# Kernel optimization log

Measured on AMD Instinct MI355X. Metric: run time of the kernel, lower is better.

Reference implementation:

```python
import jax, jax.numpy as jnp
import numpy as np
import math

NH = 16
SIGMA = 1.5
KS = 7


def _gaussian_blur_16x16(x):
    # x: (N, 16, 16); torchvision GaussianBlur(7, 1.5) with reflect padding
    hx = jnp.arange(KS, dtype=x.dtype) - (KS - 1) / 2.0
    k1 = jnp.exp(-0.5 * (hx / SIGMA) ** 2)
    k1 = k1 / k1.sum()
    k2 = jnp.outer(k1, k1)[None, None]  # (1,1,7,7)
    pad = KS // 2
    xp = jnp.pad(x, ((0, 0), (pad, pad), (pad, pad)), mode='reflect')[:, None]
    y = jax.lax.conv_general_dilated(xp, k2, (1, 1), 'VALID')
    return y[:, 0]


def _normalize(w):
    mn, mx = w.min(), w.max()
    return (w - mn) / (mx - mn)


def _blurred_map(f, b_perm):
    # f, b_perm: (B, 256, 256)
    B = f.shape[0]
    bi = f * b_perm
    bi = bi.reshape(B * 256, 16, 16)
    bl = _gaussian_blur_16x16(bi)
    bl = jnp.clip(_normalize(bl), 0.0, 1.0)
    bl = bl.reshape(B, 256, 256)
    return bl * f * b_perm


def setup_inputs() -> dict:
    key = jax.random.key(0)
    ks = jax.random.split(key, 16)
    B, T, C = 4, 827, 1024
    inp = {
        'x': jax.random.normal(ks[0], (B, T, C), jnp.float32),
        'h': jax.random.normal(ks[1], (B, NH, 827, 827), jnp.float32) * 0.1,
        'f01': jax.random.uniform(ks[2], (B, 256, 256), jnp.float32),
        'f02': jax.random.uniform(ks[3], (B, 256, 256), jnp.float32),
        'f12': jax.random.uniform(ks[4], (B, 256, 256), jnp.float32),
        'b01': jax.random.uniform(ks[5], (B, 256, 256), jnp.float32),
        'b02': jax.random.uniform(ks[6], (B, 256, 256), jnp.float32),
        'b12': jax.random.uniform(ks[7], (B, 256, 256), jnp.float32),
        'Wq': jax.random.normal(ks[8], (C, C), jnp.float32) * 0.02,
        'bq': jnp.zeros((C,), jnp.float32),
        'Wk': jax.random.normal(ks[9], (C, C), jnp.float32) * 0.02,
        'bk': jnp.zeros((C,), jnp.float32),
        'Wv': jax.random.normal(ks[10], (C, C), jnp.float32) * 0.02,
        'bv': jnp.zeros((C,), jnp.float32),
        'Wp': jax.random.normal(ks[11], (C, C), jnp.float32) * 0.02,
        'bp': jnp.zeros((C,), jnp.float32),
    }
    return inp


def reference(x, h, f01, f02, f12, b01, b02, b12,
              Wq, bq, Wk, bk, Wv, bv, Wp, bp):
    B, T, C = x.shape
    hd = C // NH
    # QKV projections -> (B, NH, T, hd)
    def proj(W, b):
        return (x @ W + b).reshape(B, T, NH, hd).transpose(0, 2, 1, 3)
    q, k, v = proj(Wq, bq), proj(Wk, bk), proj(Wv, bv)

    att = jnp.einsum('bhtd,bhsd->bhts', q, k) * (1.0 / math.sqrt(hd))
    att = h[:, :, :T, :T] + att  # adaptive additive bias

    # bidirectional epipolar multiplicative masks with blur
    b01p = jnp.transpose(b01, (0, 2, 1))
    b02p = jnp.transpose(b02, (0, 2, 1))
    b12p = jnp.transpose(b12, (0, 2, 1))
    blur01 = _blurred_map(f01, b01p)[:, None]  # (B,1,256,256), broadcast over heads
    blur02 = _blurred_map(f02, b02p)[:, None]
    blur12 = _blurred_map(f12, b12p)[:, None]

    n1 = min(T - 285, 256)
    att = att.at[:, :, 285:285 + n1, 0:256].multiply(blur01[:, :, :n1])
    if T > 571:
        n2 = T - 571
        att = att.at[:, :, 571:T, 0:256].multiply(blur02[:, :, :n2])
        att = att.at[:, :, 571:T, 286:542].multiply(blur12[:, :, :n2])

    mask = jnp.tril(jnp.ones((T, T), dtype=bool))
    att = jnp.where(mask, att, -jnp.inf)
    att = jax.nn.softmax(att, axis=-1)

    y = jnp.einsum('bhts,bhsd->bhtd', att, v)
    y = y.transpose(0, 2, 1, 3).reshape(B, T, C)
    return y @ Wp + bp
```

## Files before the change

### kernel.cpp

```cpp
#include <hip/hip_runtime.h>
#include <math.h>

using bfrag8 = __attribute__((ext_vector_type(8))) short;
using facc4  = __attribute__((ext_vector_type(4))) float;

#define MFMA16(a,b,c) __builtin_amdgcn_mfma_f32_16x16x32_bf16((a),(b),(c),0,0,0)

#define T_SEQ 827
#define T_PAD 832
#define NHEAD 16
#define NEG_INF (-__builtin_inff())
#define CM_TOT 1179392

static __device__ __forceinline__ unsigned short f2bf(float f) {
    unsigned int x = __float_as_uint(f);
    unsigned int r = x + 0x7FFFu + ((x >> 16) & 1u);
    return (unsigned short)(r >> 16);
}

static __device__ __forceinline__ void gl16(const void* g, void* l) {
    __builtin_amdgcn_global_load_lds(
        (const __attribute__((address_space(1))) unsigned int*)g,
        (__attribute__((address_space(3))) unsigned int*)l,
        16, 0, 0);
}

__global__ __launch_bounds__(256) void k_front(const float* __restrict__ x,
                                               unsigned short* __restrict__ x_bf,
                                               float* __restrict__ cm,
                                               unsigned short* q, unsigned short* k,
                                               unsigned short* vT,
                                               const float* __restrict__ Wq,
                                               const float* __restrict__ Wk,
                                               const float* __restrict__ Wv,
                                               const float* __restrict__ Wp,
                                               unsigned short* __restrict__ Wt_out,
                                               const float* f01, const float* f02, const float* f12,
                                               const float* b01, const float* b02, const float* b12,
                                               float* __restrict__ bl,
                                               float* __restrict__ pmm) {
    __shared__ float tile[32][33];
    __shared__ float img[16][17], tmp[16][17];
    __shared__ float smn[4], smx[4];
    int bid = blockIdx.x, tid = threadIdx.x;

    if (bid < 3308) {
        int i = (bid * 256 + tid) * 4;
        float4 v = *reinterpret_cast<const float4*>(x + i);
        ushort4 o;
        o.x = f2bf(v.x); o.y = f2bf(v.y); o.z = f2bf(v.z); o.w = f2bf(v.w);
        *reinterpret_cast<ushort4*>(x_bf + i) = o;
    } else if (bid < 4460) {
        int base = (bid - 3308) * 1024 + tid * 4;
        if (base + 4 <= CM_TOT) {
            float4 one = {1.f, 1.f, 1.f, 1.f};
            *reinterpret_cast<float4*>(cm + base) = one;
        } else {
#pragma unroll
            for (int j = 0; j < 4; ++j)
                if (base + j < CM_TOT) cm[base + j] = 1.f;
        }
    } else if (bid < 4524) {
        int bh = bid - 4460;
        for (int i = tid; i < 320; i += 256) {
            int t = 827 + i / 64, d = i % 64;
            q[((size_t)bh * T_PAD + t) * 64 + d] = 0;
            k[((size_t)bh * T_PAD + t) * 64 + d] = 0;
        }
        for (int i = tid; i < 4096; i += 256) {
            int d = i >> 6, s = 768 + (i & 63);
            vT[((size_t)bh * 64 + d) * T_PAD + s] = 0;
        }
    } else if (bid < 8620) {
        int i = bid - 4524;
        int z = i >> 10, rem = i & 1023;
        int bx = rem & 31, by = rem >> 5;
        const float* W = (z == 0) ? Wq : (z == 1) ? Wk : (z == 2) ? Wv : Wp;
        unsigned short* Wt = Wt_out + (size_t)z * 1048576;
        int tx = tid & 31, ty0 = tid >> 5;
#pragma unroll
        for (int j = 0; j < 4; ++j) {
            int ty = ty0 + j * 8;
            tile[ty][tx] = W[(size_t)(by * 32 + ty) * 1024 + bx * 32 + tx];
        }
        __syncthreads();
#pragma unroll
        for (int j = 0; j < 4; ++j) {
            int ty = ty0 + j * 8;
            Wt[(size_t)(bx * 32 + ty) * 1024 + by * 32 + tx] = f2bf(tile[tx][ty]);
        }
    } else {
        int i = bid - 8620;
        int m = i >> 10, rem = i & 1023, b = rem >> 8, r = rem & 255;
        const float* f  = (m == 0) ? f01 : (m == 1) ? f02 : f12;
        const float* bm = (m == 0) ? b01 : (m == 1) ? b02 : b12;
        int ii = tid >> 4, j = tid & 15;

        float k1[7]; float ks = 0.f;
#pragma unroll
        for (int d = 0; d < 7; ++d) { float hx = (float)d - 3.f; k1[d] = expf(-0.5f * hx * hx / 2.25f); ks += k1[d]; }
#pragma unroll
        for (int d = 0; d < 7; ++d) k1[d] /= ks;

        size_t idx = (size_t)b * 65536 + (size_t)r * 256 + tid;
        float bi = f[idx] * bm[(size_t)b * 65536 + (size_t)tid * 256 + r];
        img[ii][j] = bi;
        __syncthreads();
        float ha = 0.f;
#pragma unroll
        for (int d = 0; d < 7; ++d) { int p = j - 3 + d; p = p < 0 ? -p : (p > 15 ? 30 - p : p); ha += k1[d] * img[ii][p]; }
        tmp[ii][j] = ha;
        __syncthreads();
        float v = 0.f;
#pragma unroll
        for (int d = 0; d < 7; ++d) { int p = ii - 3 + d; p = p < 0 ? -p : (p > 15 ? 30 - p : p); v += k1[d] * tmp[p][j]; }
        bl[(size_t)m * 262144 + idx] = v;

        float mn = v, mx = v;
#pragma unroll
        for (int off = 32; off; off >>= 1) { mn = fminf(mn, __shfl_xor(mn, off)); mx = fmaxf(mx, __shfl_xor(mx, off)); }
        int wid = tid >> 6, lane = tid & 63;
        if (lane == 0) { smn[wid] = mn; smx[wid] = mx; }
        __syncthreads();
        if (tid == 0) {
            mn = fminf(fminf(smn[0], smn[1]), fminf(smn[2], smn[3]));
            mx = fmaxf(fmaxf(smx[0], smx[1]), fmaxf(smx[2], smx[3]));
            pmm[2 * i]     = mn;
            pmm[2 * i + 1] = mx;
        }
    }
}

__global__ __launch_bounds__(256) void k_gemm_qkv(const unsigned short* __restrict__ A,
                                              const unsigned short* __restrict__ Bt,
                                              const float* __restrict__ b0, const float* __restrict__ b1,
                                              const float* __restrict__ b2,
                                              unsigned short* __restrict__ qo, unsigned short* __restrict__ ko,
                                              unsigned short* __restrict__ vo, int M,
                                              const float* f01, const float* f02, const float* f12,
                                              const float* b01, const float* b02, const float* b12,
                                              const float* __restrict__ bl,
                                              const float* __restrict__ pmm,
                                              float* __restrict__ cm) {
    __shared__ unsigned short As[2][4096];
    __shared__ unsigned short Bs[2][4096];
    int bid = blockIdx.x, tid = threadIdx.x;

    if (bid >= 624) {
        int i = bid - 624;
        int m = i >> 10, rem = i & 1023, b = rem >> 8, r = rem & 255;
        float mn = __builtin_inff(), mx = 0.f;
        for (int kk = tid; kk < 1024; kk += 256) {
            int e = m * 1024 + kk;
            mn = fminf(mn, pmm[2 * e]);
            mx = fmaxf(mx, pmm[2 * e + 1]);
        }
#pragma unroll
        for (int off = 32; off; off >>= 1) { mn = fminf(mn, __shfl_xor(mn, off)); mx = fmaxf(mx, __shfl_xor(mx, off)); }
        float* fs = reinterpret_cast<float*>(&As[0][0]);
        int wid = tid >> 6, lane = tid & 63;
        if (lane == 0) { fs[wid] = mn; fs[4 + wid] = mx; }
        __syncthreads();
        mn = fminf(fminf(fs[0], fs[1]), fminf(fs[2], fs[3]));
        mx = fmaxf(fmaxf(fs[4], fs[5]), fmaxf(fs[6], fs[7]));

        const float* f  = (m == 0) ? f01 : (m == 1) ? f02 : f12;
        const float* bm = (m == 0) ? b01 : (m == 1) ? b02 : b12;
        size_t idx = (size_t)b * 65536 + (size_t)r * 256 + tid;
        float w = (bl[(size_t)m * 262144 + idx] - mn) / (mx - mn);
        w = fminf(fmaxf(w, 0.f), 1.f);
        float val = w * f[idx] * bm[(size_t)b * 65536 + (size_t)tid * 256 + r];
        int row = (m == 0) ? r : r + 286;
        int col = (m == 2) ? tid + 286 : tid;
        cm[((size_t)b * 542 + row) * 544 + col] = val;
        return;
    }

    int swz = (bid & 7) * 78 + (bid >> 3);
    int m0 = (swz % 26) * 128, n0 = (swz / 26) * 128;
    int wid = tid >> 6, lane = tid & 63;
    int g = lane >> 4, l15 = lane & 15;
    int wm = wid >> 1, wn = wid & 1;
    facc4 acc[4][4] = {};

    int ar0 = m0 + (tid >> 2); if (ar0 > M - 1) ar0 = M - 1;
    int ar1 = m0 + 64 + (tid >> 2); if (ar1 > M - 1) ar1 = M - 1;
    const unsigned short* Ap0 = A + (size_t)ar0 * 1024 + (tid & 3) * 8;
    const unsigned short* Ap1 = A + (size_t)ar1 * 1024 + (tid & 3) * 8;
    const unsigned short* Bp0 = Bt + (size_t)(n0 + (tid >> 2)) * 1024 + (tid & 3) * 8;
    const unsigned short* Bp1 = Bp0 + (size_t)64 * 1024;

    auto stage = [&](int koff, int buf) {
        gl16(Ap0 + koff, &As[buf][0] + (wid << 9));
        gl16(Ap1 + koff, &As[buf][0] + (wid << 9) + 2048);
        gl16(Bp0 + koff, &Bs[buf][0] + (wid << 9));
        gl16(Bp1 + koff, &Bs[buf][0] + (wid << 9) + 2048);
    };

    stage(0, 0);
    for (int k0 = 0; k0 < 32; ++k0) {
        int cur = k0 & 1;
        bool morek = (k0 + 1 < 32);
        if (morek) {
            stage((k0 + 1) * 32, cur ^ 1);
            asm volatile("s_waitcnt vmcnt(4)" ::: "memory");
        } else {
            asm volatile("s_waitcnt vmcnt(0)" ::: "memory");
        }
        __builtin_amdgcn_s_barrier();
        __builtin_amdgcn_sched_barrier(0);

        bfrag8 af[4], bf[4];
#pragma unroll
        for (int mi = 0; mi < 4; ++mi)
            af[mi] = *reinterpret_cast<const bfrag8*>(&As[cur][(wm * 64 + mi * 16 + l15) * 32 + g * 8]);
#pragma unroll
        for (int ni = 0; ni < 4; ++ni)
            bf[ni] = *reinterpret_cast<const bfrag8*>(&Bs[cur][(wn * 64 + ni * 16 + l15) * 32 + g * 8]);
        __builtin_amdgcn_s_setprio(1);
#pragma unroll
        for (int mi = 0; mi < 4; ++mi)
#pragma unroll
            for (int ni = 0; ni < 4; ++ni)
                acc[mi][ni] = MFMA16(af[mi], bf[ni], acc[mi][ni]);
        __builtin_amdgcn_s_setprio(0);

        __builtin_amdgcn_sched_barrier(0);
        if (morek) __builtin_amdgcn_s_barrier();
    }

    int which = n0 >> 10;
    const float* bb = (which == 0 ? b0 : (which == 1 ? b1 : b2));
#pragma unroll
    for (int mi = 0; mi < 4; ++mi)
#pragma unroll
        for (int ni = 0; ni < 4; ++ni)
#pragma unroll
            for (int r = 0; r < 4; ++r) {
                int row = m0 + wm * 64 + mi * 16 + g * 4 + r;
                if (row >= M) continue;
                int col = n0 + wn * 64 + ni * 16 + l15;
                float v = acc[mi][ni][r] + bb[col & 1023];
                int b = row / T_SEQ, t = row - b * T_SEQ;
                int cc = col & 1023;
                int hh = cc >> 6, d = cc & 63;
                size_t bh = (size_t)(b * NHEAD + hh);
                if (which == 0) {
                    qo[(bh * T_PAD + t) * 64 + d] = f2bf(v);
                } else if (which == 1) {
                    int du = (((d >> 3) ^ (t & 7)) << 3) | (d & 7);
                    ko[(bh * T_PAD + t) * 64 + du] = f2bf(v);
                } else {
                    int sl = t & 63;
                    int su = (((sl >> 3) ^ (d & 7)) << 3) | (t & 7);
                    vo[(bh * 64 + d) * T_PAD + (t - sl) + su] = f2bf(v);
                }
            }
}

__global__ __launch_bounds__(256) void k_proj64(const unsigned short* __restrict__ A,
                                                const unsigned short* __restrict__ Bt,
                                                const float* __restrict__ bias,
                                                float* __restrict__ out, int M) {
    __shared__ unsigned short As[2048];
    __shared__ unsigned short Bs[2048];
    int bid = blockIdx.x, tid = threadIdx.x;
    int swz = (bid & 7) * 104 + (bid >> 3);
    int m0 = (swz % 52) * 64, n0 = (swz / 52) * 64;
    int wid = tid >> 6, lane = tid & 63;
    int g = lane >> 4, l15 = lane & 15;
    int wm = wid >> 1, wn = wid & 1;
    facc4 acc[2][2] = {};

    int ar = m0 + (tid >> 2); if (ar > M - 1) ar = M - 1;
    const unsigned short* Ap = A + (size_t)ar * 1024 + (tid & 3) * 8;
    const unsigned short* Bp = Bt + (size_t)(n0 + (tid >> 2)) * 1024 + (tid & 3) * 8;
    unsigned short* asw = As + (wid << 9);
    unsigned short* bsw = Bs + (wid << 9);

    for (int k0 = 0; k0 < 1024; k0 += 32) {
        if (k0) __syncthreads();
        gl16(Ap + k0, asw);
        gl16(Bp + k0, bsw);
        __syncthreads();
        bfrag8 af[2], bf[2];
#pragma unroll
        for (int mi = 0; mi < 2; ++mi)
            af[mi] = *reinterpret_cast<const bfrag8*>(&As[(wm * 32 + mi * 16 + l15) * 32 + g * 8]);
#pragma unroll
        for (int ni = 0; ni < 2; ++ni)
            bf[ni] = *reinterpret_cast<const bfrag8*>(&Bs[(wn * 32 + ni * 16 + l15) * 32 + g * 8]);
#pragma unroll
        for (int mi = 0; mi < 2; ++mi)
#pragma unroll
            for (int ni = 0; ni < 2; ++ni)
                acc[mi][ni] = MFMA16(af[mi], bf[ni], acc[mi][ni]);
    }

#pragma unroll
    for (int mi = 0; mi < 2; ++mi)
#pragma unroll
        for (int ni = 0; ni < 2; ++ni)
#pragma unroll
            for (int r = 0; r < 4; ++r) {
                int row = m0 + wm * 32 + mi * 16 + g * 4 + r;
                if (row >= M) continue;
                int col = n0 + wn * 32 + ni * 16 + l15;
                out[(size_t)row * 1024 + col] = acc[mi][ni][r] + bias[col];
            }
}

__global__ __launch_bounds__(256) void k_attn(const unsigned short* __restrict__ qb,
                                              const unsigned short* __restrict__ kb,
                                              const unsigned short* __restrict__ vT,
                                              const float* __restrict__ h,
                                              const float* __restrict__ cm,
                                              unsigned short* __restrict__ y) {
    int blk0 = blockIdx.x;
    int blk = (blk0 & 7) * 104 + (blk0 >> 3);
    int bh = blk / 13;
    int qt = 12 - (blk % 13);
    int b = bh >> 4, hh = bh & 15;
    int tid = threadIdx.x, wid = tid >> 6, lane = tid & 63;
    int g = lane >> 4, l15 = lane & 15;
    int t0 = qt * 64 + wid * 16;
    int t = t0 + l15;
    int tcl = t > 826 ? 826 : t;
    int ntiles = qt + 1;

    __shared__ unsigned short Ks[2][4096];
    __shared__ unsigned short Vs[2][4096];
    __shared__ unsigned short Ps[4][1024];
    unsigned short* pw = &Ps[wid][0];

    const unsigned short* Kbase = kb + (size_t)bh * T_PAD * 64;
    const unsigned short* Vbase = vT + (size_t)bh * 64 * T_PAD;
    const float* hrow = h + (size_t)bh * T_SEQ * T_SEQ + (size_t)tcl * T_SEQ;
    int rt = t - 285; rt = rt < 0 ? 0 : (rt > 541 ? 541 : rt);
    const float* cmrow = cm + ((size_t)b * 542 + rt) * 544;
    bool tm = (t >= 285);

    size_t qrow = ((size_t)bh * T_PAD + t) * 64 + g * 8;
    bfrag8 aq0 = *reinterpret_cast<const bfrag8*>(qb + qrow);
    bfrag8 aq1 = *reinterpret_cast<const bfrag8*>(qb + qrow + 32);

    auto stage = [&](int s0, int buf) {
        const unsigned short* kt = Kbase + (size_t)s0 * 64;
        unsigned short* kd = &Ks[buf][0] + (wid << 9);
        gl16(kt + tid * 8, kd);
        gl16(kt + 2048 + tid * 8, kd + 2048);
        const unsigned short* vt = Vbase + s0;
        unsigned short* vd = &Vs[buf][0] + (wid << 9);
        gl16(vt + (size_t)(tid >> 3) * T_PAD + (tid & 7) * 8, vd);
        gl16(vt + (size_t)((tid >> 3) + 32) * T_PAD + (tid & 7) * 8, vd + 2048);
    };

    auto loadh = [&](int s0t, float* hv, float* mv) {
#pragma unroll
        for (int nt = 0; nt < 4; ++nt) {
            int sb = s0t + nt * 16 + 4 * g;
            float h4[4];
            if (sb + 3 <= tcl) {
                __builtin_memcpy(h4, hrow + sb, 16);
            } else {
#pragma unroll
                for (int j = 0; j < 4; ++j) {
                    float hx = 0.f;
                    if (sb + j <= tcl) hx = hrow[sb + j];
                    h4[j] = hx;
                }
            }
            float m4[4];
            if (tm && sb <= 540) {
                __builtin_memcpy(m4, cmrow + sb, 16);
            } else {
#pragma unroll
                for (int j = 0; j < 4; ++j) m4[j] = 1.f;
            }
#pragma unroll
            for (int j = 0; j < 4; ++j) { hv[nt * 4 + j] = h4[j]; mv[nt * 4 + j] = m4[j]; }
        }
    };

    float m_r = NEG_INF, l_r = 0.f;
    facc4 acc[4] = {};
    float hv[16], mv[16];
    loadh(0, hv, mv);
    stage(0, 0);

    for (int it = 0; it < ntiles; ++it) {
        int cur = it & 1, s0 = it * 64;
        bool more = (it + 1 < ntiles);
        bool diag = !more;
        __syncthreads();
        if (more) stage(s0 + 64, cur ^ 1);

        facc4 sf[4] = {};
        __builtin_amdgcn_s_setprio(1);
#pragma unroll
        for (int nt = 0; nt < 4; ++nt) {
            int row = nt * 16 + l15;
            const unsigned short* kp = &Ks[cur][row * 64];
            bfrag8 k0 = *reinterpret_cast<const bfrag8*>(kp + ((g ^ (row & 7)) << 3));
            bfrag8 k1 = *reinterpret_cast<const bfrag8*>(kp + (((4 + g) ^ (row & 7)) << 3));
            sf[nt] = MFMA16(k0, aq0, sf[nt]);
            sf[nt] = MFMA16(k1, aq1, sf[nt]);
        }
        __builtin_amdgcn_s_setprio(0);

        float vmax = NEG_INF;
#pragma unroll
        for (int nt = 0; nt < 4; ++nt)
#pragma unroll
            for (int r = 0; r < 4; ++r) {
                float val = fmaf(sf[nt][r], 0.125f, hv[nt * 4 + r]) * mv[nt * 4 + r];
                if (diag) {
                    int s = s0 + nt * 16 + 4 * g + r;
                    val = (s <= tcl) ? val : NEG_INF;
                }
                sf[nt][r] = val;
                vmax = fmaxf(vmax, val);
            }

        if (more) loadh(s0 + 64, hv, mv);

        vmax = fmaxf(vmax, __shfl_xor(vmax, 16));
        vmax = fmaxf(vmax, __shfl_xor(vmax, 32));

        bool noresc = __all(vmax <= m_r + 6.0f);
        float mnew = fmaxf(m_r, vmax);
        float mexp = noresc ? m_r : mnew;

        float ps = 0.f;
#pragma unroll
        for (int nt = 0; nt < 4; ++nt)
#pragma unroll
            for (int r = 0; r < 4; ++r) {
                float p = __expf(sf[nt][r] - mexp);
                sf[nt][r] = p;
                ps += p;
            }
        ps += __shfl_xor(ps, 16);
        ps += __shfl_xor(ps, 32);

#pragma unroll
        for (int nt = 0; nt < 4; ++nt) {
            unsigned u0, u1;
            asm("v_cvt_pk_bf16_f32 %0, %1, %2" : "=v"(u0) : "v"(sf[nt][0]), "v"(sf[nt][1]));
            asm("v_cvt_pk_bf16_f32 %0, %1, %2" : "=v"(u1) : "v"(sf[nt][2]), "v"(sf[nt][3]));
            int el = (l15 * 64 + nt * 16 + 4 * g) ^ ((l15 & 7) << 3);
            uint2 uu; uu.x = u0; uu.y = u1;
            *reinterpret_cast<uint2*>(&pw[el]) = uu;
        }

        if (!noresc) {
            float scale = __expf(m_r - mnew);
            l_r = l_r * scale + ps;
#pragma unroll
            for (int r = 0; r < 4; ++r) {
                float sc = __int_as_float(__builtin_amdgcn_ds_bpermute((4 * g + r) * 4, __float_as_int(scale)));
#pragma unroll
                for (int dt = 0; dt < 4; ++dt) acc[dt][r] *= sc;
            }
            m_r = mnew;
        } else {
            l_r += ps;
        }

        __builtin_amdgcn_s_setprio(1);
#pragma unroll
        for (int c2 = 0; c2 < 2; ++c2) {
            int ela = (l15 * 64 + c2 * 32 + 8 * g) ^ ((l15 & 7) << 3);
            bfrag8 ap = *reinterpret_cast<const bfrag8*>(&pw[ela]);
#pragma unroll
            for (int dt = 0; dt < 4; ++dt) {
                int row = dt * 16 + l15;
                bfrag8 vf = *reinterpret_cast<const bfrag8*>(&Vs[cur][row * 64 + (((c2 * 4 + g) ^ (row & 7)) << 3)]);
                acc[dt] = MFMA16(ap, vf, acc[dt]);
            }
        }
        __builtin_amdgcn_s_setprio(0);
    }

    float linv = 1.0f / l_r;
#pragma unroll
    for (int r = 0; r < 4; ++r) {
        float li = __int_as_float(__builtin_amdgcn_ds_bpermute((4 * g + r) * 4, __float_as_int(linv)));
        int tt = t0 + 4 * g + r;
        if (tt < T_SEQ) {
#pragma unroll
            for (int dt = 0; dt < 4; ++dt)
                y[((size_t)(b * T_SEQ) + tt) * 1024 + hh * 64 + dt * 16 + l15] = f2bf(acc[dt][r] * li);
        }
    }
}

extern "C" void kernel_launch(void* const* d_in, const int* in_sizes, int n_in,
                              void* d_out, int out_size, void* d_ws, size_t ws_size,
                              hipStream_t stream) {
    const float* x   = (const float*)d_in[0];
    const float* h   = (const float*)d_in[1];
    const float* f01 = (const float*)d_in[2];
    const float* f02 = (const float*)d_in[3];
    const float* f12 = (const float*)d_in[4];
    const float* b01 = (const float*)d_in[5];
    const float* b02 = (const float*)d_in[6];
    const float* b12 = (const float*)d_in[7];
    const float* Wq  = (const float*)d_in[8];
    const float* bq  = (const float*)d_in[9];
    const float* Wk  = (const float*)d_in[10];
    const float* bk  = (const float*)d_in[11];
    const float* Wv  = (const float*)d_in[12];
    const float* bv  = (const float*)d_in[13];
    const float* Wp  = (const float*)d_in[14];
    const float* bp  = (const float*)d_in[15];

    char* ws = (char*)d_ws;
    float* pmm    = (float*)(ws + 256);
    float* bl     = (float*)(ws + 256 + 24576);
    float* cmb    = (float*)(ws + 256 + 24576 + 3145728);
    unsigned short* x_bf  = (unsigned short*)(ws + 256 + 24576 + 3145728 + 4717568);
    unsigned short* WtQKV = x_bf + (size_t)3308 * 1024;
    unsigned short* WtP   = WtQKV + (size_t)3072 * 1024;
    unsigned short* q_bf  = WtP + (size_t)1024 * 1024;
    unsigned short* k_bf  = q_bf + (size_t)64 * T_PAD * 64;
    unsigned short* vTb   = k_bf + (size_t)64 * T_PAD * 64;
    unsigned short* y_bf  = vTb  + (size_t)64 * T_PAD * 64;

    k_front<<<11692, 256, 0, stream>>>(x, x_bf, cmb, q_bf, k_bf, vTb,
                                       Wq, Wk, Wv, Wp, WtQKV,
                                       f01, f02, f12, b01, b02, b12, bl, pmm);
    k_gemm_qkv<<<3696, 256, 0, stream>>>(x_bf, WtQKV, bq, bk, bv, q_bf, k_bf, vTb, 3308,
                                         f01, f02, f12, b01, b02, b12, bl, pmm, cmb);
    k_attn<<<832, 256, 0, stream>>>(q_bf, k_bf, vTb, h, cmb, y_bf);
    k_proj64<<<832, 256, 0, stream>>>(y_bf, WtP, bp, (float*)d_out, 3308);
}
```

Measured before the change: 133.3 us.

## Split long causal attention query tiles across two blocks with a combine pass

For query tiles 7-12, the attention kernel now splits the key range into two halves, each processed by its own block. The partial accumulators and running max/sum are written to workspace and merged flash-decoding style in a new k_combine kernel. This balances the triangular causal workload and raises the block count from 832 to 1216 to shorten the tail. In exchange it adds an extra launch, fp32 partial-result traffic, and reuse of the x_bf and bl workspace regions as scratch.

New measurement: 135.9 us. No clear change (+2.0%).

```diff
diff --git a/kernel.cpp b/kernel.cpp
--- a/kernel.cpp
+++ b/kernel.cpp
@@ -315,18 +315,29 @@
                                               const unsigned short* __restrict__ vT,
                                               const float* __restrict__ h,
                                               const float* __restrict__ cm,
-                                              unsigned short* __restrict__ y) {
+                                              unsigned short* __restrict__ y,
+                                              float* __restrict__ pacc,
+                                              float* __restrict__ pml) {
     int blk0 = blockIdx.x;
-    int blk = (blk0 & 7) * 104 + (blk0 >> 3);
-    int bh = blk / 13;
-    int qt = 12 - (blk % 13);
+    int swz = (blk0 & 7) * 152 + (blk0 >> 3);
+    int bh = swz / 19, j = swz % 19;
+    int qt, itlo, ithi, pidx = -1;
+    if (j < 7) {
+        qt = j; itlo = 0; ithi = qt + 1;
+    } else {
+        qt = 7 + ((j - 7) >> 1);
+        int half = (j - 7) & 1;
+        int h0 = (qt + 2) >> 1;
+        itlo = half ? h0 : 0;
+        ithi = half ? (qt + 1) : h0;
+        pidx = bh * 12 + (qt - 7) * 2 + half;
+    }
     int b = bh >> 4, hh = bh & 15;
     int tid = threadIdx.x, wid = tid >> 6, lane = tid & 63;
     int g = lane >> 4, l15 = lane & 15;
     int t0 = qt * 64 + wid * 16;
     int t = t0 + l15;
     int tcl = t > 826 ? 826 : t;
-    int ntiles = qt + 1;
 
     __shared__ unsigned short Ks[2][4096];
     __shared__ unsigned short Vs[2][4096];
@@ -364,10 +375,10 @@
                 __builtin_memcpy(h4, hrow + sb, 16);
             } else {
 #pragma unroll
-                for (int j = 0; j < 4; ++j) {
+                for (int jj = 0; jj < 4; ++jj) {
                     float hx = 0.f;
-                    if (sb + j <= tcl) hx = hrow[sb + j];
-                    h4[j] = hx;
+                    if (sb + jj <= tcl) hx = hrow[sb + jj];
+                    h4[jj] = hx;
                 }
             }
             float m4[4];
@@ -375,23 +386,23 @@
                 __builtin_memcpy(m4, cmrow + sb, 16);
             } else {
 #pragma unroll
-                for (int j = 0; j < 4; ++j) m4[j] = 1.f;
-            }
-#pragma unroll
-            for (int j = 0; j < 4; ++j) { hv[nt * 4 + j] = h4[j]; mv[nt * 4 + j] = m4[j]; }
+                for (int jj = 0; jj < 4; ++jj) m4[jj] = 1.f;
+            }
+#pragma unroll
+            for (int jj = 0; jj < 4; ++jj) { hv[nt * 4 + jj] = h4[jj]; mv[nt * 4 + jj] = m4[jj]; }
         }
     };
 
     float m_r = NEG_INF, l_r = 0.f;
     facc4 acc[4] = {};
     float hv[16], mv[16];
-    loadh(0, hv, mv);
-    stage(0, 0);
-
-    for (int it = 0; it < ntiles; ++it) {
-        int cur = it & 1, s0 = it * 64;
-        bool more = (it + 1 < ntiles);
-        bool diag = !more;
+    loadh(itlo * 64, hv, mv);
+    stage(itlo * 64, 0);
+
+    for (int it = itlo; it < ithi; ++it) {
+        int cur = (it - itlo) & 1, s0 = it * 64;
+        bool more = (it + 1 < ithi);
+        bool diag = (it == qt);
         __syncthreads();
         if (more) stage(s0 + 64, cur ^ 1);
 
@@ -482,16 +493,62 @@
         __builtin_amdgcn_s_setprio(0);
     }
 
-    float linv = 1.0f / l_r;
-#pragma unroll
-    for (int r = 0; r < 4; ++r) {
-        float li = __int_as_float(__builtin_amdgcn_ds_bpermute((4 * g + r) * 4, __float_as_int(linv)));
-        int tt = t0 + 4 * g + r;
-        if (tt < T_SEQ) {
-#pragma unroll
-            for (int dt = 0; dt < 4; ++dt)
-                y[((size_t)(b * T_SEQ) + tt) * 1024 + hh * 64 + dt * 16 + l15] = f2bf(acc[dt][r] * li);
-        }
+    if (pidx < 0) {
+        float linv = 1.0f / l_r;
+#pragma unroll
+        for (int r = 0; r < 4; ++r) {
+            float li = __int_as_float(__builtin_amdgcn_ds_bpermute((4 * g + r) * 4, __float_as_int(linv)));
+            int tt = t0 + 4 * g + r;
+            if (tt < T_SEQ) {
+#pragma unroll
+                for (int dt = 0; dt < 4; ++dt)
+                    y[((size_t)(b * T_SEQ) + tt) * 1024 + hh * 64 + dt * 16 + l15] = f2bf(acc[dt][r] * li);
+            }
+        }
+    } else {
+        float* pa = pacc + (size_t)pidx * 4096;
+        float* pm = pml + (size_t)pidx * 128;
+        if (g == 0) {
+            int prow = wid * 16 + l15;
+            pm[prow * 2]     = m_r;
+            pm[prow * 2 + 1] = l_r;
+        }
+#pragma unroll
+        for (int dt = 0; dt < 4; ++dt)
+#pragma unroll
+            for (int r = 0; r < 4; ++r)
+                pa[(wid * 16 + 4 * g + r) * 64 + dt * 16 + l15] = acc[dt][r];
+    }
+}
+
+__global__ __launch_bounds__(256) void k_combine(const float* __restrict__ pacc,
+                                                 const float* __restrict__ pml,
+                                                 unsigned short* __restrict__ y) {
+    int blk = blockIdx.x;
+    int bh = blk / 6, qi = blk % 6;
+    int qt = 7 + qi;
+    int b = bh >> 4, hh = bh & 15;
+    int p0 = bh * 12 + qi * 2, p1 = p0 + 1;
+    int tid = threadIdx.x;
+    int row = tid >> 2;
+    int c0 = (tid & 3) * 16;
+
+    float m0 = pml[(size_t)p0 * 128 + row * 2],     l0 = pml[(size_t)p0 * 128 + row * 2 + 1];
+    float m1 = pml[(size_t)p1 * 128 + row * 2],     l1 = pml[(size_t)p1 * 128 + row * 2 + 1];
+    float m  = fmaxf(m0, m1);
+    float s0 = __expf(m0 - m), s1 = __expf(m1 - m);
+    float inv = 1.0f / (l0 * s0 + l1 * s1);
+
+    int tt = qt * 64 + row;
+    if (tt >= T_SEQ) return;
+    const float* a0 = pacc + (size_t)p0 * 4096 + row * 64;
+    const float* a1 = pacc + (size_t)p1 * 4096 + row * 64;
+    unsigned short* yo = y + ((size_t)(b * T_SEQ) + tt) * 1024 + hh * 64;
+#pragma unroll
+    for (int jj = 0; jj < 16; ++jj) {
+        int col = c0 + jj;
+        float v = (a0[col] * s0 + a1[col] * s1) * inv;
+        yo[col] = f2bf(v);
     }
 }
 
@@ -527,11 +584,15 @@
     unsigned short* vTb   = k_bf + (size_t)64 * T_PAD * 64;
     unsigned short* y_bf  = vTb  + (size_t)64 * T_PAD * 64;
 
+    float* pacc = (float*)x_bf;
+    float* pml  = bl;
+
     k_front<<<11692, 256, 0, stream>>>(x, x_bf, cmb, q_bf, k_bf, vTb,
                                        Wq, Wk, Wv, Wp, WtQKV,
                                        f01, f02, f12, b01, b02, b12, bl, pmm);
     k_gemm_qkv<<<3696, 256, 0, stream>>>(x_bf, WtQKV, bq, bk, bv, q_bf, k_bf, vTb, 3308,
                                          f01, f02, f12, b01, b02, b12, bl, pmm, cmb);
-    k_attn<<<832, 256, 0, stream>>>(q_bf, k_bf, vTb, h, cmb, y_bf);
+    k_attn<<<1216, 256, 0, stream>>>(q_bf, k_bf, vTb, h, cmb, y_bf, pacc, pml);
+    k_combine<<<384, 256, 0, stream>>>(pacc, pml, y_bf);
     k_proj64<<<832, 256, 0, stream>>>(y_bf, WtP, bp, (float*)d_out, 3308);
 }
```
